# Kernel tuning notes

Measured on AMD Instinct MI355X. Metric: run time of the kernel, lower is better.

Reference implementation:

```python
import jax, jax.numpy as jnp
import numpy as np

D_MODEL = 1024
N_HEADS = 16
HEAD_DIM = D_MODEL // N_HEADS


def setup_inputs() -> dict:
    key = jax.random.key(0)
    ks = jax.random.split(key, 9)
    s = 0.02
    return {
        "x": jax.random.normal(ks[0], (2, 2048, D_MODEL), jnp.float32),
        "Wk": jax.random.normal(ks[1], (D_MODEL, D_MODEL), jnp.float32) * s,
        "bk": jnp.zeros((D_MODEL,), jnp.float32),
        "Wq": jax.random.normal(ks[2], (D_MODEL, D_MODEL), jnp.float32) * s,
        "bq": jnp.zeros((D_MODEL,), jnp.float32),
        "Wv": jax.random.normal(ks[3], (D_MODEL, D_MODEL), jnp.float32) * s,
        "bv": jnp.zeros((D_MODEL,), jnp.float32),
        "Wp": jax.random.normal(ks[4], (D_MODEL, D_MODEL), jnp.float32) * s,
        "bp": jnp.zeros((D_MODEL,), jnp.float32),
    }


def reference(x, Wk, bk, Wq, bq, Wv, bv, Wp, bp):
    B, T, C = x.shape
    H, Dh = N_HEADS, HEAD_DIM
    # linear projections; torch Linear: y = x @ W.T + b
    def split_heads(y):
        return y.reshape(B, T, H, Dh).transpose(0, 2, 1, 3)  # [B,H,T,Dh]
    k = split_heads(x @ Wk.T + bk)
    q = split_heads(x @ Wq.T + bq)
    v = split_heads(x @ Wv.T + bv)
    scale = 1.0 / jnp.sqrt(jnp.asarray(Dh, x.dtype))
    att = jnp.einsum("bhqd,bhkd->bhqk", q, k) * scale  # [B,H,T,T]
    causal = jnp.tril(jnp.ones((T, T), bool))
    att = jnp.where(causal[None, None], att, -jnp.inf)
    att = jax.nn.softmax(att, axis=-1)
    y = jnp.einsum("bhqk,bhkd->bhqd", att, v)  # [B,H,T,Dh]
    y = y.transpose(0, 2, 1, 3).reshape(B, T, C)
    return y @ Wp.T + bp
```

## Files before the change

### kernel.cpp

```cpp
#include <hip/hip_runtime.h>
#include <stdint.h>

typedef unsigned short u16;
typedef __bf16 bf16x8_t __attribute__((ext_vector_type(8)));
typedef float f32x4 __attribute__((ext_vector_type(4)));

#define T_LEN 2048
#define NHEADS 16
#define DHEAD 64
#define DMODEL 1024
#define QSCALE 0.1803368801111f

__device__ __forceinline__ u16 f2bf(float f) {
  union { float f; uint32_t u; } v; v.f = f;
  uint32_t r = v.u + 0x7FFFu + ((v.u >> 16) & 1u);
  return (u16)(r >> 16);
}

__device__ __forceinline__ void gload16(const u16* g, u16* l) {
  __builtin_amdgcn_global_load_lds((const __attribute__((address_space(1))) void*)g,
                                   (__attribute__((address_space(3))) void*)l, 16, 0, 0);
}

__global__ void cvt_bf16_k(const float* __restrict__ s, u16* __restrict__ d, int n) {
  int i = (blockIdx.x * blockDim.x + threadIdx.x) * 4;
  if (i >= n) return;
  float4 f = *(const float4*)(s + i);
  u16 o[4] = { f2bf(f.x), f2bf(f.y), f2bf(f.z), f2bf(f.w) };
  *(uint2*)(d + i) = *(const uint2*)o;
}

__global__ void cvt_w_k(const float* __restrict__ wq, const float* __restrict__ wk,
                        const float* __restrict__ wv, const float* __restrict__ wp,
                        u16* __restrict__ dqkv, u16* __restrict__ dp) {
  int which = blockIdx.y;
  const float* s = which == 0 ? wq : (which == 1 ? wk : (which == 2 ? wv : wp));
  u16* d = which == 3 ? dp : dqkv + (size_t)which * 1048576;
  int i = (blockIdx.x * blockDim.x + threadIdx.x) * 4;
  float4 f = *(const float4*)(s + i);
  u16 o[4] = { f2bf(f.x), f2bf(f.y), f2bf(f.z), f2bf(f.w) };
  *(uint2*)(d + i) = *(const uint2*)o;
}

template <int TM, int TN, int MODE>
__global__ __launch_bounds__(256, 3) void gemm_k(
    const u16* __restrict__ A, const u16* __restrict__ Bw,
    const float* __restrict__ b0, const float* __restrict__ b1, const float* __restrict__ b2,
    void* __restrict__ o0, void* __restrict__ o1, void* __restrict__ o2,
    int M, int N, int K)
{
  __shared__ __align__(16) u16 As[TM][64];
  __shared__ __align__(16) u16 Bs[TN][64];
  const int m0 = blockIdx.x * TM, n0 = blockIdx.y * TN;
  const int tid = threadIdx.x, lane = tid & 63, w = tid >> 6;
  const int col = lane & 15, quad = lane >> 4;
  constexpr int WM = TM / 2, WN = TN / 2;
  const int wm = (w >> 1) * WM, wn = (w & 1) * WN;
  constexpr int NI = WM / 16, NJ = WN / 16;
  const int rsub = lane >> 3;
  const int csw = ((lane & 7) ^ rsub) * 8;
  const int rx8 = col & 7;

  f32x4 acc[NI][NJ] = {};

  for (int k0 = 0; k0 < K; k0 += 64) {
    __syncthreads();
#pragma unroll
    for (int i = 0; i < TM / 32; i++) {
      int rb = (i * 4 + w) * 8;
      gload16(&A[(size_t)(m0 + rb + rsub) * K + k0 + csw], &As[rb][0]);
    }
#pragma unroll
    for (int i = 0; i < TN / 32; i++) {
      int rb = (i * 4 + w) * 8;
      gload16(&Bw[(size_t)(n0 + rb + rsub) * K + k0 + csw], &Bs[rb][0]);
    }
    __syncthreads();
#pragma unroll
    for (int s = 0; s < 2; s++) {
      bf16x8_t af[NI], bfr[NJ];
#pragma unroll
      for (int i = 0; i < NI; i++) {
        int cp = (quad ^ rx8) ^ (s * 4);
        af[i] = *(const bf16x8_t*)&As[wm + i * 16 + col][cp * 8];
      }
#pragma unroll
      for (int j = 0; j < NJ; j++) {
        int cp = (quad ^ rx8) ^ (s * 4);
        bfr[j] = *(const bf16x8_t*)&Bs[wn + j * 16 + col][cp * 8];
      }
#pragma unroll
      for (int i = 0; i < NI; i++)
#pragma unroll
        for (int j = 0; j < NJ; j++)
          acc[i][j] = __builtin_amdgcn_mfma_f32_16x16x32_bf16(af[i], bfr[j], acc[i][j], 0, 0, 0);
    }
  }

#pragma unroll
  for (int i = 0; i < NI; i++) {
#pragma unroll
    for (int j = 0; j < NJ; j++) {
      int ncol = n0 + wn + j * 16 + col;
      if (MODE == 0) {
        float bias = b0[ncol];
#pragma unroll
        for (int r = 0; r < 4; r++) {
          int m = m0 + wm + i * 16 + quad * 4 + r;
          ((float*)o0)[(size_t)m * N + ncol] = acc[i][j][r] + bias;
        }
      } else {
        int sect = ncol >> 10, nc = ncol & 1023;
        const float* bp = sect == 0 ? b0 : (sect == 1 ? b1 : b2);
        u16* op = sect == 0 ? (u16*)o0 : (sect == 1 ? (u16*)o1 : (u16*)o2);
        float bias = bp[nc];
        float scal = sect == 0 ? QSCALE : 1.0f;
        int h = nc >> 6, d = nc & 63;
#pragma unroll
        for (int r = 0; r < 4; r++) {
          int m = m0 + wm + i * 16 + quad * 4 + r;
          int b = m >> 11, t = m & 2047;
          float v = (acc[i][j][r] + bias) * scal;
          size_t idx = sect < 2 ? ((((size_t)(b * NHEADS + h)) * T_LEN + t) * DHEAD + d)
                                : ((((size_t)(b * NHEADS + h)) * DHEAD + d) * T_LEN + t);
          op[idx] = f2bf(v);
        }
      }
    }
  }
}

__global__ __launch_bounds__(256, 3) void attn_k(
    const u16* __restrict__ Q, const u16* __restrict__ Kb,
    const u16* __restrict__ Vt, u16* __restrict__ Y)
{
  __shared__ __align__(16) u16 Ks[2][64][64];
  __shared__ __align__(16) u16 Vs[2][64][64];
  __shared__ __align__(16) u16 Ps[4][16][68];
  const int bid = blockIdx.x;
  const int bh = (bid & 7) * 4 + ((bid >> 3) & 3);
  const int qt = 31 - (bid >> 5);
  const int tid = threadIdx.x, lane = tid & 63, w = tid >> 6;
  const int col = lane & 15, quad = lane >> 4;
  const int b = bh >> 4, h = bh & 15;
  const int qw = qt * 64 + w * 16;

  const int rsub = lane >> 3;
  const int csw = ((lane & 7) ^ rsub) * 8;
  const u16* kgb = Kb + (size_t)bh * T_LEN * DHEAD;
  const u16* vgb = Vt + (size_t)bh * DHEAD * T_LEN;
  const int rx = col & 7;

  bf16x8_t qf0, qf1;
  {
    const u16* p = Q + ((size_t)bh * T_LEN + qw + col) * DHEAD + quad * 8;
    qf0 = *(const bf16x8_t*)p;
    qf1 = *(const bf16x8_t*)(p + 32);
  }

  float lsum[4] = {0.f, 0.f, 0.f, 0.f};
  f32x4 o[4] = {};
  int qrow[4];
#pragma unroll
  for (int r = 0; r < 4; r++) qrow[r] = qw + quad * 4 + r;

#pragma unroll
  for (int half = 0; half < 2; half++) {
    int rb = w * 16 + half * 8;
    gload16(kgb + (size_t)(rb + rsub) * DHEAD + csw, &Ks[0][rb][0]);
    gload16(vgb + (size_t)(rb + rsub) * T_LEN + csw, &Vs[0][rb][0]);
  }

  for (int kt = 0; kt <= qt; ++kt) {
    const int k0 = kt * 64;
    const int bufi = kt & 1;
    __syncthreads();
    if (kt < qt) {
      const int k0n = k0 + 64, bn = bufi ^ 1;
#pragma unroll
      for (int half = 0; half < 2; half++) {
        int rb = w * 16 + half * 8;
        gload16(kgb + (size_t)(k0n + rb + rsub) * DHEAD + csw, &Ks[bn][rb][0]);
        gload16(vgb + (size_t)(rb + rsub) * T_LEN + k0n + csw, &Vs[bn][rb][0]);
      }
    }

    f32x4 s[4];
#pragma unroll
    for (int nt = 0; nt < 4; nt++) {
      const u16* krow = &Ks[bufi][nt * 16 + col][0];
      bf16x8_t kf0 = *(const bf16x8_t*)(krow + ((quad ^ rx) & 7) * 8);
      bf16x8_t kf1 = *(const bf16x8_t*)(krow + (((4 + quad) ^ rx) & 7) * 8);
      f32x4 a = {};
      a = __builtin_amdgcn_mfma_f32_16x16x32_bf16(qf0, kf0, a, 0, 0, 0);
      a = __builtin_amdgcn_mfma_f32_16x16x32_bf16(qf1, kf1, a, 0, 0, 0);
      s[nt] = a;
    }

    const bool diag = (kt == qt);
#pragma unroll
    for (int r = 0; r < 4; r++) {
#pragma unroll
      for (int nt = 0; nt < 4; nt++) {
        float p = __builtin_amdgcn_exp2f(s[nt][r]);
        if (diag && (k0 + nt * 16 + col) > qrow[r]) p = 0.f;
        uint32_t pu = __float_as_uint(p) & 0xFFFF0000u;
        lsum[r] += __uint_as_float(pu);
        Ps[w][quad * 4 + r][nt * 16 + col] = (u16)(pu >> 16);
      }
    }

#pragma unroll
    for (int ks = 0; ks < 2; ks++) {
      bf16x8_t pf = *(const bf16x8_t*)&Ps[w][col][ks * 32 + quad * 8];
#pragma unroll
      for (int dt = 0; dt < 4; dt++) {
        const u16* vrow = &Vs[bufi][dt * 16 + col][0];
        bf16x8_t vv = *(const bf16x8_t*)(vrow + (((ks * 4 + quad) ^ rx) & 7) * 8);
        o[dt] = __builtin_amdgcn_mfma_f32_16x16x32_bf16(pf, vv, o[dt], 0, 0, 0);
      }
    }
  }

#pragma unroll
  for (int r = 0; r < 4; r++) {
#pragma unroll
    for (int off = 1; off < 16; off <<= 1)
      lsum[r] += __shfl_xor(lsum[r], off);
    float inv = 1.0f / lsum[r];
    int t = qw + quad * 4 + r;
#pragma unroll
    for (int dt = 0; dt < 4; dt++)
      Y[((size_t)(b * T_LEN + t)) * DMODEL + h * DHEAD + dt * 16 + col] =
          f2bf(o[dt][r] * inv);
  }
}

extern "C" void kernel_launch(void* const* d_in, const int* in_sizes, int n_in,
                              void* d_out, int out_size, void* d_ws, size_t ws_size,
                              hipStream_t stream) {
  const float* x  = (const float*)d_in[0];
  const float* Wk = (const float*)d_in[1];
  const float* bk = (const float*)d_in[2];
  const float* Wq = (const float*)d_in[3];
  const float* bq = (const float*)d_in[4];
  const float* Wv = (const float*)d_in[5];
  const float* bv = (const float*)d_in[6];
  const float* Wp = (const float*)d_in[7];
  const float* bp = (const float*)d_in[8];

  char* ws = (char*)d_ws;
  const size_t MB = 1u << 20;
  u16* xb    = (u16*)(ws);
  u16* wqkv  = (u16*)(ws + 8 * MB);
  u16* wpb   = (u16*)(ws + 14 * MB);
  u16* qb    = (u16*)(ws + 16 * MB);
  u16* kb    = (u16*)(ws + 24 * MB);
  u16* vtb   = (u16*)(ws + 32 * MB);
  u16* yatt  = (u16*)(ws + 40 * MB);

  cvt_bf16_k<<<4096, 256, 0, stream>>>(x, xb, 4194304);
  dim3 gw(1024, 4);
  cvt_w_k<<<gw, 256, 0, stream>>>(Wq, Wk, Wv, Wp, wqkv, wpb);

  dim3 gqkv(32, 24);
  gemm_k<128, 128, 3><<<gqkv, 256, 0, stream>>>(xb, wqkv, bq, bk, bv,
                                                qb, kb, vtb, 4096, 3072, 1024);

  attn_k<<<1024, 256, 0, stream>>>(qb, kb, vtb, yatt);

  dim3 gp(32, 16);
  gemm_k<128, 64, 0><<<gp, 256, 0, stream>>>(yatt, wpb, bp, nullptr, nullptr,
                                             d_out, nullptr, nullptr, 4096, 1024, 1024);
}
```

Baseline: 177.2 us.

## Process 128-row query tiles per block with 32 rows per wave

Each attention block now covers 128 query rows instead of 64, and each wave handles two 16-row query subtiles that share every K and V fragment loaded from LDS. The grid is halved to 512 blocks, and waves skip KV tiles beyond their own causal diagonal. This doubles the MFMA work per K/V LDS read and halves global K/V traffic per query row. The cost is more registers, a larger P buffer, and load imbalance because half the waves sit idle on the last KV tile.

```diff
diff --git a/kernel.cpp b/kernel.cpp
--- a/kernel.cpp
+++ b/kernel.cpp
@@ -136,14 +136,16 @@
 {
   __shared__ __align__(16) u16 Ks[2][64][64];
   __shared__ __align__(16) u16 Vs[2][64][64];
-  __shared__ __align__(16) u16 Ps[4][16][68];
+  __shared__ __align__(16) u16 Ps[4][32][68];
   const int bid = blockIdx.x;
   const int bh = (bid & 7) * 4 + ((bid >> 3) & 3);
-  const int qt = 31 - (bid >> 5);
+  const int qj = 15 - (bid >> 5);
   const int tid = threadIdx.x, lane = tid & 63, w = tid >> 6;
   const int col = lane & 15, quad = lane >> 4;
   const int b = bh >> 4, h = bh & 15;
-  const int qw = qt * 64 + w * 16;
+  const int qw = qj * 128 + w * 32;
+  const int ktop = 2 * qj + 1;
+  const int ktw = 2 * qj + (w >> 1);
 
   const int rsub = lane >> 3;
   const int csw = ((lane & 7) ^ rsub) * 8;
@@ -151,18 +153,16 @@
   const u16* vgb = Vt + (size_t)bh * DHEAD * T_LEN;
   const int rx = col & 7;
 
-  bf16x8_t qf0, qf1;
-  {
-    const u16* p = Q + ((size_t)bh * T_LEN + qw + col) * DHEAD + quad * 8;
-    qf0 = *(const bf16x8_t*)p;
-    qf1 = *(const bf16x8_t*)(p + 32);
-  }
-
-  float lsum[4] = {0.f, 0.f, 0.f, 0.f};
-  f32x4 o[4] = {};
-  int qrow[4];
-#pragma unroll
-  for (int r = 0; r < 4; r++) qrow[r] = qw + quad * 4 + r;
+  bf16x8_t qf[2][2];
+#pragma unroll
+  for (int s2 = 0; s2 < 2; s2++) {
+    const u16* p = Q + ((size_t)bh * T_LEN + qw + s2 * 16 + col) * DHEAD + quad * 8;
+    qf[s2][0] = *(const bf16x8_t*)p;
+    qf[s2][1] = *(const bf16x8_t*)(p + 32);
+  }
+
+  float lsum[2][4] = {};
+  f32x4 o[2][4] = {};
 
 #pragma unroll
   for (int half = 0; half < 2; half++) {
@@ -171,11 +171,11 @@
     gload16(vgb + (size_t)(rb + rsub) * T_LEN + csw, &Vs[0][rb][0]);
   }
 
-  for (int kt = 0; kt <= qt; ++kt) {
+  for (int kt = 0; kt <= ktop; ++kt) {
     const int k0 = kt * 64;
     const int bufi = kt & 1;
     __syncthreads();
-    if (kt < qt) {
+    if (kt < ktop) {
       const int k0n = k0 + 64, bn = bufi ^ 1;
 #pragma unroll
       for (int half = 0; half < 2; half++) {
@@ -184,55 +184,71 @@
         gload16(vgb + (size_t)(rb + rsub) * T_LEN + k0n + csw, &Vs[bn][rb][0]);
       }
     }
-
-    f32x4 s[4];
+    if (kt > ktw) continue;
+
+    f32x4 s[2][4];
 #pragma unroll
     for (int nt = 0; nt < 4; nt++) {
       const u16* krow = &Ks[bufi][nt * 16 + col][0];
       bf16x8_t kf0 = *(const bf16x8_t*)(krow + ((quad ^ rx) & 7) * 8);
       bf16x8_t kf1 = *(const bf16x8_t*)(krow + (((4 + quad) ^ rx) & 7) * 8);
-      f32x4 a = {};
-      a = __builtin_amdgcn_mfma_f32_16x16x32_bf16(qf0, kf0, a, 0, 0, 0);
-      a = __builtin_amdgcn_mfma_f32_16x16x32_bf16(qf1, kf1, a, 0, 0, 0);
-      s[nt] = a;
-    }
-
-    const bool diag = (kt == qt);
-#pragma unroll
-    for (int r = 0; r < 4; r++) {
-#pragma unroll
-      for (int nt = 0; nt < 4; nt++) {
-        float p = __builtin_amdgcn_exp2f(s[nt][r]);
-        if (diag && (k0 + nt * 16 + col) > qrow[r]) p = 0.f;
-        uint32_t pu = __float_as_uint(p) & 0xFFFF0000u;
-        lsum[r] += __uint_as_float(pu);
-        Ps[w][quad * 4 + r][nt * 16 + col] = (u16)(pu >> 16);
+#pragma unroll
+      for (int s2 = 0; s2 < 2; s2++) {
+        f32x4 a = {};
+        a = __builtin_amdgcn_mfma_f32_16x16x32_bf16(qf[s2][0], kf0, a, 0, 0, 0);
+        a = __builtin_amdgcn_mfma_f32_16x16x32_bf16(qf[s2][1], kf1, a, 0, 0, 0);
+        s[s2][nt] = a;
+      }
+    }
+
+    const bool diag = (kt == ktw);
+#pragma unroll
+    for (int s2 = 0; s2 < 2; s2++) {
+#pragma unroll
+      for (int r = 0; r < 4; r++) {
+        const int qrow = qw + s2 * 16 + quad * 4 + r;
+#pragma unroll
+        for (int nt = 0; nt < 4; nt++) {
+          float p = __builtin_amdgcn_exp2f(s[s2][nt][r]);
+          if (diag && (k0 + nt * 16 + col) > qrow) p = 0.f;
+          uint32_t pu = __float_as_uint(p) & 0xFFFF0000u;
+          lsum[s2][r] += __uint_as_float(pu);
+          Ps[w][s2 * 16 + quad * 4 + r][nt * 16 + col] = (u16)(pu >> 16);
+        }
       }
     }
 
 #pragma unroll
     for (int ks = 0; ks < 2; ks++) {
-      bf16x8_t pf = *(const bf16x8_t*)&Ps[w][col][ks * 32 + quad * 8];
+      bf16x8_t pf[2];
+#pragma unroll
+      for (int s2 = 0; s2 < 2; s2++)
+        pf[s2] = *(const bf16x8_t*)&Ps[w][s2 * 16 + col][ks * 32 + quad * 8];
 #pragma unroll
       for (int dt = 0; dt < 4; dt++) {
         const u16* vrow = &Vs[bufi][dt * 16 + col][0];
         bf16x8_t vv = *(const bf16x8_t*)(vrow + (((ks * 4 + quad) ^ rx) & 7) * 8);
-        o[dt] = __builtin_amdgcn_mfma_f32_16x16x32_bf16(pf, vv, o[dt], 0, 0, 0);
-      }
-    }
-  }
-
-#pragma unroll
-  for (int r = 0; r < 4; r++) {
-#pragma unroll
-    for (int off = 1; off < 16; off <<= 1)
-      lsum[r] += __shfl_xor(lsum[r], off);
-    float inv = 1.0f / lsum[r];
-    int t = qw + quad * 4 + r;
-#pragma unroll
-    for (int dt = 0; dt < 4; dt++)
-      Y[((size_t)(b * T_LEN + t)) * DMODEL + h * DHEAD + dt * 16 + col] =
-          f2bf(o[dt][r] * inv);
+#pragma unroll
+        for (int s2 = 0; s2 < 2; s2++)
+          o[s2][dt] = __builtin_amdgcn_mfma_f32_16x16x32_bf16(pf[s2], vv, o[s2][dt], 0, 0, 0);
+      }
+    }
+  }
+
+#pragma unroll
+  for (int s2 = 0; s2 < 2; s2++) {
+#pragma unroll
+    for (int r = 0; r < 4; r++) {
+#pragma unroll
+      for (int off = 1; off < 16; off <<= 1)
+        lsum[s2][r] += __shfl_xor(lsum[s2][r], off);
+      float inv = 1.0f / lsum[s2][r];
+      int t = qw + s2 * 16 + quad * 4 + r;
+#pragma unroll
+      for (int dt = 0; dt < 4; dt++)
+        Y[((size_t)(b * T_LEN + t)) * DMODEL + h * DHEAD + dt * 16 + col] =
+            f2bf(o[s2][dt][r] * inv);
+    }
   }
 }
 
@@ -267,7 +283,7 @@
   gemm_k<128, 128, 3><<<gqkv, 256, 0, stream>>>(xb, wqkv, bq, bk, bv,
                                                 qb, kb, vtb, 4096, 3072, 1024);
 
-  attn_k<<<1024, 256, 0, stream>>>(qb, kb, vtb, yatt);
+  attn_k<<<512, 256, 0, stream>>>(qb, kb, vtb, yatt);
 
   dim3 gp(32, 16);
   gemm_k<128, 64, 0><<<gp, 256, 0, stream>>>(yatt, wpb, bp, nullptr, nullptr,
```

Result: slower. 197.8 us (+11.6%).
